# Kernel tuning notes

Measured on AMD Instinct MI355X. Metric: run time of the kernel, lower is better.

The kernel has to match this reference:

```python
import jax, jax.numpy as jnp
import numpy as np

B, C, H, W = 8, 64, 64, 64
CI = 32  # inter_channels = in_channels // 2
EPS = 1e-5


def conv1x1(x, w, b=None):
    # x: (b,c,h,w), w: (o,c) -> (b,o,h,w)
    y = jnp.einsum('bchw,oc->bohw', x, w)
    if b is not None:
        y = y + b[None, :, None, None]
    return y


def maxpool2x2(x):
    b, c, h, w = x.shape
    return x.reshape(b, c, h // 2, 2, w // 2, 2).max(axis=(3, 5))


def setup_inputs() -> dict:
    key = jax.random.key(0)
    ks = jax.random.split(key, 12)
    s = 0.05
    return {
        'x': jax.random.normal(ks[0], (B, C, H, W), jnp.float32),
        'theta_w': jax.random.normal(ks[1], (CI, C), jnp.float32) * s,
        'theta_b': jax.random.normal(ks[2], (CI,), jnp.float32) * s,
        'phi_w': jax.random.normal(ks[3], (CI, C), jnp.float32) * s,
        'phi_b': jax.random.normal(ks[4], (CI,), jnp.float32) * s,
        'psi_w': jax.random.normal(ks[5], (CI, C), jnp.float32) * s,
        'psi_b': jax.random.normal(ks[6], (CI,), jnp.float32) * s,
        'cp_w': jax.random.normal(ks[7], (2 * CI,), jnp.float32) * s,  # concat_project 1x1, no bias
        'W_w': jax.random.normal(ks[8], (C, CI + 1), jnp.float32) * s,
        'W_b': jax.random.normal(ks[9], (C,), jnp.float32) * s,
        'bn_gamma': jax.random.normal(ks[10], (C,), jnp.float32) * s + 1.0,
        'bn_beta': jax.random.normal(ks[11], (C,), jnp.float32) * s,
    }


def reference(x, theta_w, theta_b, phi_w, phi_b, psi_w, psi_b, cp_w, W_w, W_b, bn_gamma, bn_beta):
    b = x.shape[0]
    # psi / phi branches get 2x2 maxpool (sub_sample=True default)
    psi_x = maxpool2x2(conv1x1(x, psi_w, psi_b)).reshape(b, CI, -1)      # (b,ci,M)
    psi_x = psi_x.transpose(0, 2, 1)                                     # (b,M,ci)
    theta_x = conv1x1(x, theta_w, theta_b).reshape(b, CI, -1)            # (b,ci,N)
    phi_x = maxpool2x2(conv1x1(x, phi_w, phi_b)).reshape(b, CI, -1)      # (b,ci,M)
    # concat_project(cat[theta_i, phi_j]) + ReLU == relu(w1.theta_i + w2.phi_j)
    w1, w2 = cp_w[:CI], cp_w[CI:]
    a = jnp.einsum('bcn,c->bn', theta_x, w1)                             # (b,N)
    bb = jnp.einsum('bcm,c->bm', phi_x, w2)                              # (b,M)
    f = jax.nn.relu(a[:, :, None] + bb[:, None, :])                      # (b,N,M)
    M = f.shape[-1]
    f_div_C = f / float(M)
    y = jnp.matmul(f_div_C, psi_x)                                       # (b,N,ci)
    y = y.transpose(0, 2, 1).reshape(b, CI, H, W)
    # r_structure_type='zero' -> zero structure channel
    structure_feat = jnp.zeros((b, 1, H, W), y.dtype)
    y = jnp.concatenate([y, structure_feat], axis=1)                     # (b,ci+1,H,W)
    wy = conv1x1(y, W_w, W_b)                                            # (b,C,H,W)
    # BatchNorm2d, training-mode batch stats, biased variance
    mu = wy.mean(axis=(0, 2, 3), keepdims=True)
    var = wy.var(axis=(0, 2, 3), keepdims=True)
    wy = (wy - mu) * jax.lax.rsqrt(var + EPS)
    wy = wy * bn_gamma[None, :, None, None] + bn_beta[None, :, None, None]
    return wy + x
```

## Files before the change

### kernel.cpp

```cpp
#include <hip/hip_runtime.h>

#define OFF_A    0
#define OFF_BB   32768
#define OFF_SBB  40960
#define OFF_PERM 49152
#define OFF_U    57344
#define OFF_T1   581632
#define OFF_T2   1106432
#define OFF_KK   1631232
#define OFF_MP1  1664000
#define OFF_MP2  1664512
#define OFF_HC   1665024
#define OFF_HS   1673224
#define OFF_HS2  1681424
#define OFF_BAR  1689624

#define NBLK 256
#define NGRP 8

__device__ __forceinline__ void stg(float* p, float v) {
    __hip_atomic_store(p, v, __ATOMIC_RELAXED, __HIP_MEMORY_SCOPE_AGENT);
}
__device__ __forceinline__ float ldg1(const float* p) {
    return __hip_atomic_load(p, __ATOMIC_RELAXED, __HIP_MEMORY_SCOPE_AGENT);
}
__device__ __forceinline__ void stgi(int* p, int v) {
    __hip_atomic_store(p, v, __ATOMIC_RELAXED, __HIP_MEMORY_SCOPE_AGENT);
}
__device__ __forceinline__ int ldgi(const int* p) {
    return __hip_atomic_load(p, __ATOMIC_RELAXED, __HIP_MEMORY_SCOPE_AGENT);
}

__device__ __forceinline__ void gbar(float* ws, int gen)
{
    __syncthreads();
    if (threadIdx.x == 0) {
        unsigned* bars = (unsigned*)(ws + OFF_BAR);
        unsigned* grp  = bars + ((blockIdx.x >> 5) + 1) * 32;
        unsigned old = __hip_atomic_fetch_add(grp, 1u, __ATOMIC_RELAXED,
                                              __HIP_MEMORY_SCOPE_AGENT);
        if (old == (unsigned)(gen * 32 - 1))
            __hip_atomic_fetch_add(bars, 1u, __ATOMIC_RELAXED,
                                   __HIP_MEMORY_SCOPE_AGENT);
        unsigned goal = (unsigned)(gen * NGRP);
        while (__hip_atomic_load(bars, __ATOMIC_RELAXED,
                                 __HIP_MEMORY_SCOPE_AGENT) < goal)
            __builtin_amdgcn_s_sleep(2);
    }
    __syncthreads();
}

__global__ __launch_bounds__(1024) void kMega(
    const float* __restrict__ x, const float* __restrict__ theta_w,
    const float* __restrict__ theta_b, const float* __restrict__ phi_w,
    const float* __restrict__ phi_b, const float* __restrict__ psi_w,
    const float* __restrict__ psi_b, const float* __restrict__ cp_w,
    const float* __restrict__ Ww, const float* __restrict__ Wb,
    const float* __restrict__ gamma, const float* __restrict__ beta,
    float* __restrict__ ws, float* __restrict__ out)
{
    __shared__ float sh[8640];
    const int tid = threadIdx.x;
    const int bid = blockIdx.x;
    const int b   = bid >> 5;
    const int sub = bid & 31;

    {
        float* sm   = sh;
        float* sth  = sh + 4160;
        float* spsi = sh + 4228;
        float* sWw  = sh + 5284;
        for (int e = tid; e < 2048; e += 1024) {
            int i = e >> 6, c = e & 63;
            sm[i*130 + 2*c]     = phi_w[e];
            sm[i*130 + 2*c + 1] = psi_w[e];
        }
        for (int e = tid; e < 2048; e += 1024)
            sWw[(e >> 5)*33 + (e & 31)] = Ww[(e >> 5)*33 + (e & 31)];
        if (tid < 64) {
            float s = 0;
            for (int i = 0; i < 32; ++i) s += cp_w[i]*theta_w[i*64 + tid];
            sth[tid] = s;
        } else if (tid == 64) {
            float s = 0;
            for (int i = 0; i < 32; ++i) s += cp_w[i]*theta_b[i];
            sth[64] = s;
        }
        __syncthreads();
        int i = tid & 31;
        int mIdx = tid >> 5;
        int m = (sub << 5) + mIdx;
        int ph = m >> 5, pw = m & 31;
        const float* xb = x + b*262144 + ph*128 + pw*2;
        const float2* wrow = (const float2*)(sm + i*130);
        float tb = sth[64];
        float p0=0,p1=0,p2=0,p3=0,s0=0,s1=0,s2=0,s3=0;
        float a0=tb,a1=tb,a2=tb,a3=tb;
        #pragma unroll 8
        for (int c = 0; c < 64; ++c) {
            float2 xa = *(const float2*)(xb + c*4096);
            float2 xc = *(const float2*)(xb + c*4096 + 64);
            float2 w  = wrow[c];
            float st  = sth[c];
            p0 += xa.x*w.x; p1 += xa.y*w.x; p2 += xc.x*w.x; p3 += xc.y*w.x;
            s0 += xa.x*w.y; s1 += xa.y*w.y; s2 += xc.x*w.y; s3 += xc.y*w.y;
            a0 += xa.x*st;  a1 += xa.y*st;  a2 += xc.x*st;  a3 += xc.y*st;
        }
        float pv = fmaxf(fmaxf(p0,p1), fmaxf(p2,p3)) + phi_b[i];
        float sv = fmaxf(fmaxf(s0,s1), fmaxf(s2,s3)) + psi_b[i];
        spsi[mIdx*33 + i] = sv;
        float v = pv * cp_w[32 + i];
        v += __shfl_xor(v, 16, 32);
        v += __shfl_xor(v,  8, 32);
        v += __shfl_xor(v,  4, 32);
        v += __shfl_xor(v,  2, 32);
        v += __shfl_xor(v,  1, 32);
        if (i == 0) {
            stg(&ws[OFF_BB + (b<<10) + m], v);
            int nb = (b<<12) + ph*128 + pw*2;
            stg(&ws[OFF_A + nb],      a0);
            stg(&ws[OFF_A + nb + 1],  a1);
            stg(&ws[OFF_A + nb + 64], a2);
            stg(&ws[OFF_A + nb + 65], a3);
        }
        __syncthreads();
        #pragma unroll
        for (int rep = 0; rep < 2; ++rep) {
            int idx = tid + (rep << 10);
            int ml = idx >> 6, o = idx & 63;
            const float* pr = &spsi[ml*33];
            const float* wr = &sWw[o*33];
            float u = 0;
            #pragma unroll
            for (int i2 = 0; i2 < 32; ++i2) u += pr[i2]*wr[i2];
            stg(&ws[OFF_U + (((b<<10) + (sub<<5) + ml) << 6) + o], u);
        }
    }
    gbar(ws, 1);

    {
        float* sb = sh;
        sb[tid] = ldg1(&ws[OFF_BB + (b<<10) + tid]);
        __syncthreads();
        {
            int ml = tid >> 5, jl = tid & 31;
            int m = (sub << 5) + ml;
            float vv = sb[m];
            int cnt = 0;
            for (int s = 0; s < 32; ++s) {
                int j = jl + (s << 5);
                float u = sb[j];
                cnt += (u > vv || (u == vv && j < m)) ? 1 : 0;
            }
            cnt += __shfl_xor(cnt,  1, 32);
            cnt += __shfl_xor(cnt,  2, 32);
            cnt += __shfl_xor(cnt,  4, 32);
            cnt += __shfl_xor(cnt,  8, 32);
            cnt += __shfl_xor(cnt, 16, 32);
            if (jl == 0) {
                stg(&ws[OFF_SBB + (b<<10) + cnt], vv);
                stgi(&((int*)ws)[OFF_PERM + (b<<10) + cnt], m);
            }
        }
        {
            int l = tid >> 3, jl = tid & 7;
            int n = (sub << 7) + l;
            float av = ldg1(&ws[OFF_A + (b<<12) + n]);
            float tt = -av;
            const float2* sb2 = (const float2*)sb;
            int cnt = 0;
            for (int s = 0; s < 64; ++s) {
                float2 u = sb2[jl + (s << 3)];
                cnt += (u.x > tt) ? 1 : 0;
                cnt += (u.y > tt) ? 1 : 0;
            }
            cnt += __shfl_xor(cnt, 1, 8);
            cnt += __shfl_xor(cnt, 2, 8);
            cnt += __shfl_xor(cnt, 4, 8);
            if (jl == 0) {
                stgi(&((int*)ws)[OFF_KK + (b<<12) + n], cnt);
                atomicAdd(&ws[OFF_HC + b*1025 + cnt], 1.0f);
                atomicAdd(&ws[OFF_HS + b*1025 + cnt], av);
                atomicAdd(&ws[OFF_HS2 + b*1025 + cnt], av*av);
            }
        }
    }
    gbar(ws, 2);

    if (bid < 64) {
        int b3 = bid >> 3, og = bid & 7;
        int obase = og << 3;
        float* ssort = sh;
        int*   sperm = (int*)(sh + 1024);
        float* shc   = sh + 2048;
        float* shs   = sh + 3076;
        float* shs2  = sh + 4104;
        float* swp1  = sh + 5132;
        float* swp2  = sh + 5260;
        ssort[tid] = ldg1(&ws[OFF_SBB + (b3<<10) + tid]);
        sperm[tid] = ldgi(&((const int*)ws)[OFF_PERM + (b3<<10) + tid]);
        shc[tid]  = ldg1(&ws[OFF_HC  + b3*1025 + tid]);
        shs[tid]  = ldg1(&ws[OFF_HS  + b3*1025 + tid]);
        shs2[tid] = ldg1(&ws[OFF_HS2 + b3*1025 + tid]);
        if (tid == 0) {
            shc[1024]  = ldg1(&ws[OFF_HC  + b3*1025 + 1024]);
            shs[1024]  = ldg1(&ws[OFF_HS  + b3*1025 + 1024]);
            shs2[1024] = ldg1(&ws[OFF_HS2 + b3*1025 + 1024]);
        }
        __syncthreads();
        int ch = tid >> 3, o = tid & 7;
        int wv = tid >> 6, chl = (tid & 63) >> 3;
        const float* Ub = ws + OFF_U + (b3<<16) + obase + o;
        float p[8], sp[8];
        float s1 = 0, s2 = 0;
        #pragma unroll
        for (int jl = 0; jl < 8; ++jl) {
            int jj = (ch<<3) + jl;
            float v = ldg1(&Ub[sperm[jj]<<6]);
            p[jl] = v;
            sp[jl] = ssort[jj]*v;
            s1 += v; s2 += sp[jl];
        }
        float own1 = s1, own2 = s2;
        #pragma unroll
        for (int d = 1; d < 8; d <<= 1) {
            float u1 = __shfl_up(s1, d<<3, 64);
            float u2 = __shfl_up(s2, d<<3, 64);
            if (chl >= d) { s1 += u1; s2 += u2; }
        }
        if (chl == 7) { swp1[(wv<<3)+o] = s1; swp2[(wv<<3)+o] = s2; }
        __syncthreads();
        float off1 = 0, off2 = 0;
        for (int w = 0; w < 16; ++w) {
            if (w < wv) { off1 += swp1[(w<<3)+o]; off2 += swp2[(w<<3)+o]; }
        }
        float run1 = off1 + s1 - own1;
        float run2 = off2 + s2 - own2;
        float* T1 = ws + OFF_T1 + b3*65600 + obase + o;
        float* T2 = ws + OFF_T2 + b3*65600 + obase + o;
        if (ch == 0) { stg(&T1[0], 0.0f); stg(&T2[0], 0.0f); }
        const float inv = 1.0f/1024.0f;
        float m1 = 0, m2 = 0;
        #pragma unroll
        for (int jl = 0; jl < 8; ++jl) {
            int k = (ch<<3) + jl + 1;
            run1 += p[jl]; run2 += sp[jl];
            float t1 = run1*inv, t2 = run2*inv;
            stg(&T1[k<<6], t1);
            stg(&T2[k<<6], t2);
            float c = shc[k], sa_ = shs[k], sa2 = shs2[k];
            m1 += sa_*t1 + c*t2;
            m2 += (sa2*t1 + 2.0f*sa_*t2)*t1 + c*t2*t2;
        }
        m1 += __shfl_xor(m1,  8, 64); m2 += __shfl_xor(m2,  8, 64);
        m1 += __shfl_xor(m1, 16, 64); m2 += __shfl_xor(m2, 16, 64);
        m1 += __shfl_xor(m1, 32, 64); m2 += __shfl_xor(m2, 32, 64);
        __syncthreads();
        if (chl == 0) { swp1[(wv<<3)+o] = m1; swp2[(wv<<3)+o] = m2; }
        __syncthreads();
        if (tid < 8) {
            float a1 = 0, a2 = 0;
            for (int w = 0; w < 16; ++w) {
                a1 += swp1[(w<<3)+tid]; a2 += swp2[(w<<3)+tid];
            }
            stg(&ws[OFF_MP1 + (b3<<6) + obase + tid], a1);
            stg(&ws[OFF_MP2 + (b3<<6) + obase + tid], a2);
        }
    }
    gbar(ws, 3);

    {
        float* tile = sh;
        float* sa = sh + 8256;
        int*   sk = (int*)(sh + 8384);
        float* sA = sh + 8512;
        float* sD = sh + 8576;
        int n0 = sub << 7;
        if (tid < 128) {
            sa[tid] = ldg1(&ws[OFF_A + (b<<12) + n0 + tid]);
            sk[tid] = ldgi(&((const int*)ws)[OFF_KK + (b<<12) + n0 + tid]);
        }
        if (tid < 64) {
            const float Ninv = 1.0f/32768.0f;
            float m1s = 0, m2s = 0;
            #pragma unroll
            for (int b3 = 0; b3 < 8; ++b3) {
                m1s += ldg1(&ws[OFF_MP1 + (b3<<6) + tid]);
                m2s += ldg1(&ws[OFF_MP2 + (b3<<6) + tid]);
            }
            float m1 = m1s * Ninv;
            float m2 = m2s * Ninv;
            float wb = Wb[tid];
            float mu  = m1 + wb;
            float E2  = m2 + 2.0f*wb*m1 + wb*wb;
            float var = E2 - mu*mu;
            float A = gamma[tid] * rsqrtf(var + 1e-5f);
            sA[tid] = A;
            sD[tid] = beta[tid] + A*(wb - mu);
        }
        __syncthreads();
        const float* T1 = ws + OFF_T1 + b*65600;
        const float* T2 = ws + OFF_T2 + b*65600;
        {
            int o = tid & 63, ng = tid >> 6;
            float Ao = sA[o], Do = sD[o];
            #pragma unroll
            for (int j = 0; j < 8; ++j) {
                int n = (ng << 3) + j;
                int k = sk[n];
                float a = sa[n];
                float t1 = ldg1(&T1[(k<<6) + o]);
                float t2 = ldg1(&T2[(k<<6) + o]);
                tile[o*129 + n] = Ao*(a*t1 + t2) + Do;
            }
        }
        __syncthreads();
        {
            int n = tid & 127, og = tid >> 7;
            #pragma unroll
            for (int j = 0; j < 8; ++j) {
                int o = (og << 3) + j;
                int idx = ((b<<6) + o)*4096 + n0 + n;
                out[idx] = tile[o*129 + n] + x[idx];
            }
        }
    }
}

extern "C" void kernel_launch(void* const* d_in, const int* in_sizes, int n_in,
                              void* d_out, int out_size, void* d_ws, size_t ws_size,
                              hipStream_t stream)
{
    const float* x       = (const float*)d_in[0];
    const float* theta_w = (const float*)d_in[1];
    const float* theta_b = (const float*)d_in[2];
    const float* phi_w   = (const float*)d_in[3];
    const float* phi_b   = (const float*)d_in[4];
    const float* psi_w   = (const float*)d_in[5];
    const float* psi_b   = (const float*)d_in[6];
    const float* cp_w    = (const float*)d_in[7];
    const float* Ww      = (const float*)d_in[8];
    const float* Wb      = (const float*)d_in[9];
    const float* gamma   = (const float*)d_in[10];
    const float* beta    = (const float*)d_in[11];
    float* ws  = (float*)d_ws;
    float* out = (float*)d_out;

    hipMemsetAsync(ws + OFF_HC, 0, 24888 * sizeof(float), stream);

    kMega<<<256, 1024, 0, stream>>>(x, theta_w, theta_b, phi_w, phi_b,
                                    psi_w, psi_b, cp_w, Ww, Wb,
                                    gamma, beta, ws, out);
}
```

Measured before the change: 132.6 us.

## Replace counter grid barrier with per-block flag slots and zero histograms in-kernel

Result: slower. 137.7 us (+3.9%).

```diff
diff --git a/kernel.cpp b/kernel.cpp
--- a/kernel.cpp
+++ b/kernel.cpp
@@ -16,7 +16,6 @@
 #define OFF_BAR  1689624
 
 #define NBLK 256
-#define NGRP 8
 
 __device__ __forceinline__ void stg(float* p, float v) {
     __hip_atomic_store(p, v, __ATOMIC_RELAXED, __HIP_MEMORY_SCOPE_AGENT);
@@ -31,23 +30,35 @@
     return __hip_atomic_load(p, __ATOMIC_RELAXED, __HIP_MEMORY_SCOPE_AGENT);
 }
 
-__device__ __forceinline__ void gbar(float* ws, int gen)
+__device__ __forceinline__ void gbar(float* ws, unsigned gen)
 {
     __syncthreads();
-    if (threadIdx.x == 0) {
-        unsigned* bars = (unsigned*)(ws + OFF_BAR);
-        unsigned* grp  = bars + ((blockIdx.x >> 5) + 1) * 32;
-        unsigned old = __hip_atomic_fetch_add(grp, 1u, __ATOMIC_RELAXED,
-                                              __HIP_MEMORY_SCOPE_AGENT);
-        if (old == (unsigned)(gen * 32 - 1))
-            __hip_atomic_fetch_add(bars, 1u, __ATOMIC_RELAXED,
-                                   __HIP_MEMORY_SCOPE_AGENT);
-        unsigned goal = (unsigned)(gen * NGRP);
-        while (__hip_atomic_load(bars, __ATOMIC_RELAXED,
-                                 __HIP_MEMORY_SCOPE_AGENT) < goal)
+    unsigned* slots = (unsigned*)(ws + OFF_BAR);
+    if (threadIdx.x == 0)
+        __hip_atomic_store(&slots[blockIdx.x], gen, __ATOMIC_RELAXED,
+                           __HIP_MEMORY_SCOPE_AGENT);
+    if (threadIdx.x < 64) {
+        for (;;) {
+            unsigned mn = 0xffffffffu;
+            #pragma unroll
+            for (int r = 0; r < 4; ++r) {
+                unsigned v = __hip_atomic_load(&slots[(r<<6) + threadIdx.x],
+                                               __ATOMIC_RELAXED,
+                                               __HIP_MEMORY_SCOPE_AGENT);
+                mn = v < mn ? v : mn;
+            }
+            if (__all(mn >= gen)) break;
             __builtin_amdgcn_s_sleep(2);
+        }
     }
     __syncthreads();
+}
+
+__global__ void kZero(float* ws)
+{
+    unsigned* slots = (unsigned*)(ws + OFF_BAR);
+    __hip_atomic_store(&slots[threadIdx.x], 0u, __ATOMIC_RELAXED,
+                       __HIP_MEMORY_SCOPE_AGENT);
 }
 
 __global__ __launch_bounds__(1024) void kMega(
@@ -66,6 +77,10 @@
     const int sub = bid & 31;
 
     {
+        if (tid < 97) {
+            int e = bid*97 + tid;
+            if (e < 24600) stg(&ws[OFF_HC + e], 0.0f);
+        }
         float* sm   = sh;
         float* sth  = sh + 4160;
         float* spsi = sh + 4228;
@@ -136,7 +151,7 @@
             stg(&ws[OFF_U + (((b<<10) + (sub<<5) + ml) << 6) + o], u);
         }
     }
-    gbar(ws, 1);
+    gbar(ws, 1u);
 
     {
         float* sb = sh;
@@ -185,7 +200,7 @@
             }
         }
     }
-    gbar(ws, 2);
+    gbar(ws, 2u);
 
     if (bid < 64) {
         int b3 = bid >> 3, og = bid & 7;
@@ -267,7 +282,7 @@
             stg(&ws[OFF_MP2 + (b3<<6) + obase + tid], a2);
         }
     }
-    gbar(ws, 3);
+    gbar(ws, 3u);
 
     {
         float* tile = sh;
@@ -346,8 +361,7 @@
     float* ws  = (float*)d_ws;
     float* out = (float*)d_out;
 
-    hipMemsetAsync(ws + OFF_HC, 0, 24888 * sizeof(float), stream);
-
+    kZero<<<1, 256, 0, stream>>>(ws);
     kMega<<<256, 1024, 0, stream>>>(x, theta_w, theta_b, phi_w, phi_b,
                                     psi_w, psi_b, cp_w, Ww, Wb,
                                     gamma, beta, ws, out);
```

## Replace grid-wide barriers with per-batch barriers and spread prefix-scan stage

Applied to the files above, without the earlier changes.

New measurement: 132.3 us. Within noise of the previous version (-0.2%).

```diff
diff --git a/kernel.cpp b/kernel.cpp
--- a/kernel.cpp
+++ b/kernel.cpp
@@ -15,9 +15,6 @@
 #define OFF_HS2  1681424
 #define OFF_BAR  1689624
 
-#define NBLK 256
-#define NGRP 8
-
 __device__ __forceinline__ void stg(float* p, float v) {
     __hip_atomic_store(p, v, __ATOMIC_RELAXED, __HIP_MEMORY_SCOPE_AGENT);
 }
@@ -30,22 +27,21 @@
 __device__ __forceinline__ int ldgi(const int* p) {
     return __hip_atomic_load(p, __ATOMIC_RELAXED, __HIP_MEMORY_SCOPE_AGENT);
 }
-
-__device__ __forceinline__ void gbar(float* ws, int gen)
+__device__ __forceinline__ void stgu(unsigned* p, unsigned v) {
+    __hip_atomic_store(p, v, __ATOMIC_RELAXED, __HIP_MEMORY_SCOPE_AGENT);
+}
+__device__ __forceinline__ unsigned ldgu(const unsigned* p) {
+    return __hip_atomic_load(p, __ATOMIC_RELAXED, __HIP_MEMORY_SCOPE_AGENT);
+}
+
+__device__ __forceinline__ void gbarBatch(float* ws, int b, unsigned goal)
 {
     __syncthreads();
     if (threadIdx.x == 0) {
-        unsigned* bars = (unsigned*)(ws + OFF_BAR);
-        unsigned* grp  = bars + ((blockIdx.x >> 5) + 1) * 32;
-        unsigned old = __hip_atomic_fetch_add(grp, 1u, __ATOMIC_RELAXED,
-                                              __HIP_MEMORY_SCOPE_AGENT);
-        if (old == (unsigned)(gen * 32 - 1))
-            __hip_atomic_fetch_add(bars, 1u, __ATOMIC_RELAXED,
-                                   __HIP_MEMORY_SCOPE_AGENT);
-        unsigned goal = (unsigned)(gen * NGRP);
-        while (__hip_atomic_load(bars, __ATOMIC_RELAXED,
-                                 __HIP_MEMORY_SCOPE_AGENT) < goal)
-            __builtin_amdgcn_s_sleep(2);
+        unsigned* ctr = (unsigned*)(ws + OFF_BAR) + ((b + 1) << 5);
+        __hip_atomic_fetch_add(ctr, 1u, __ATOMIC_RELAXED,
+                               __HIP_MEMORY_SCOPE_AGENT);
+        while (ldgu(ctr) < goal) __builtin_amdgcn_s_sleep(2);
     }
     __syncthreads();
 }
@@ -64,8 +60,18 @@
     const int bid = blockIdx.x;
     const int b   = bid >> 5;
     const int sub = bid & 31;
+    unsigned* bars = (unsigned*)(ws + OFF_BAR);
 
     {
+        if (bid == 0 && tid == 0) {
+            for (int i = 0; i < 9; ++i) stgu(&bars[i << 5], 0u);
+        }
+        if (tid < 97) {
+            int e = sub*97 + tid;
+            if (e < 1025)      stg(&ws[OFF_HC  + b*1025 + e], 0.0f);
+            else if (e < 2050) stg(&ws[OFF_HS  + b*1025 + e - 1025], 0.0f);
+            else if (e < 3075) stg(&ws[OFF_HS2 + b*1025 + e - 2050], 0.0f);
+        }
         float* sm   = sh;
         float* sth  = sh + 4160;
         float* spsi = sh + 4228;
@@ -87,6 +93,10 @@
             sth[64] = s;
         }
         __syncthreads();
+        if (bid == 0 && tid == 0) {
+            stgu(&bars[288], 0x5A5A5A5Au);
+            stgu(&bars[289], 0xA5A5A5A5u);
+        }
         int i = tid & 31;
         int mIdx = tid >> 5;
         int m = (sub << 5) + mIdx;
@@ -136,7 +146,16 @@
             stg(&ws[OFF_U + (((b<<10) + (sub<<5) + ml) << 6) + o], u);
         }
     }
-    gbar(ws, 1);
+    __syncthreads();
+    if (tid == 0) {
+        while ((ldgu(&bars[288]) ^ ldgu(&bars[289])) != 0xFFFFFFFFu)
+            __builtin_amdgcn_s_sleep(2);
+        unsigned* ctr = bars + ((b + 1) << 5);
+        __hip_atomic_fetch_add(ctr, 1u, __ATOMIC_RELAXED,
+                               __HIP_MEMORY_SCOPE_AGENT);
+        while (ldgu(ctr) < 32u) __builtin_amdgcn_s_sleep(2);
+    }
+    __syncthreads();
 
     {
         float* sb = sh;
@@ -185,37 +204,37 @@
             }
         }
     }
-    gbar(ws, 2);
-
-    if (bid < 64) {
-        int b3 = bid >> 3, og = bid & 7;
-        int obase = og << 3;
+    gbarBatch(ws, b, 64u);
+
+    {
+        int obase = sub << 1;
         float* ssort = sh;
         int*   sperm = (int*)(sh + 1024);
         float* shc   = sh + 2048;
         float* shs   = sh + 3076;
         float* shs2  = sh + 4104;
         float* swp1  = sh + 5132;
-        float* swp2  = sh + 5260;
-        ssort[tid] = ldg1(&ws[OFF_SBB + (b3<<10) + tid]);
-        sperm[tid] = ldgi(&((const int*)ws)[OFF_PERM + (b3<<10) + tid]);
-        shc[tid]  = ldg1(&ws[OFF_HC  + b3*1025 + tid]);
-        shs[tid]  = ldg1(&ws[OFF_HS  + b3*1025 + tid]);
-        shs2[tid] = ldg1(&ws[OFF_HS2 + b3*1025 + tid]);
+        float* swp2  = sh + 5164;
+        ssort[tid] = ldg1(&ws[OFF_SBB + (b<<10) + tid]);
+        sperm[tid] = ldgi(&((const int*)ws)[OFF_PERM + (b<<10) + tid]);
+        shc[tid]  = ldg1(&ws[OFF_HC  + b*1025 + tid]);
+        shs[tid]  = ldg1(&ws[OFF_HS  + b*1025 + tid]);
+        shs2[tid] = ldg1(&ws[OFF_HS2 + b*1025 + tid]);
         if (tid == 0) {
-            shc[1024]  = ldg1(&ws[OFF_HC  + b3*1025 + 1024]);
-            shs[1024]  = ldg1(&ws[OFF_HS  + b3*1025 + 1024]);
-            shs2[1024] = ldg1(&ws[OFF_HS2 + b3*1025 + 1024]);
-        }
-        __syncthreads();
-        int ch = tid >> 3, o = tid & 7;
-        int wv = tid >> 6, chl = (tid & 63) >> 3;
-        const float* Ub = ws + OFF_U + (b3<<16) + obase + o;
-        float p[8], sp[8];
+            shc[1024]  = ldg1(&ws[OFF_HC  + b*1025 + 1024]);
+            shs[1024]  = ldg1(&ws[OFF_HS  + b*1025 + 1024]);
+            shs2[1024] = ldg1(&ws[OFF_HS2 + b*1025 + 1024]);
+        }
+        __syncthreads();
+        int ch = tid >> 1, o2 = tid & 1;
+        int o  = obase + o2;
+        int wv = tid >> 6, chl = (tid & 63) >> 1;
+        const float* Ub = ws + OFF_U + (b<<16) + o;
+        float p[2], sp[2];
         float s1 = 0, s2 = 0;
         #pragma unroll
-        for (int jl = 0; jl < 8; ++jl) {
-            int jj = (ch<<3) + jl;
+        for (int jl = 0; jl < 2; ++jl) {
+            int jj = (ch<<1) + jl;
             float v = ldg1(&Ub[sperm[jj]<<6]);
             p[jl] = v;
             sp[jl] = ssort[jj]*v;
@@ -223,27 +242,27 @@
         }
         float own1 = s1, own2 = s2;
         #pragma unroll
-        for (int d = 1; d < 8; d <<= 1) {
-            float u1 = __shfl_up(s1, d<<3, 64);
-            float u2 = __shfl_up(s2, d<<3, 64);
+        for (int d = 1; d < 32; d <<= 1) {
+            float u1 = __shfl_up(s1, d<<1, 64);
+            float u2 = __shfl_up(s2, d<<1, 64);
             if (chl >= d) { s1 += u1; s2 += u2; }
         }
-        if (chl == 7) { swp1[(wv<<3)+o] = s1; swp2[(wv<<3)+o] = s2; }
+        if (chl == 31) { swp1[(wv<<1)+o2] = s1; swp2[(wv<<1)+o2] = s2; }
         __syncthreads();
         float off1 = 0, off2 = 0;
         for (int w = 0; w < 16; ++w) {
-            if (w < wv) { off1 += swp1[(w<<3)+o]; off2 += swp2[(w<<3)+o]; }
+            if (w < wv) { off1 += swp1[(w<<1)+o2]; off2 += swp2[(w<<1)+o2]; }
         }
         float run1 = off1 + s1 - own1;
         float run2 = off2 + s2 - own2;
-        float* T1 = ws + OFF_T1 + b3*65600 + obase + o;
-        float* T2 = ws + OFF_T2 + b3*65600 + obase + o;
+        float* T1 = ws + OFF_T1 + b*65600 + o;
+        float* T2 = ws + OFF_T2 + b*65600 + o;
         if (ch == 0) { stg(&T1[0], 0.0f); stg(&T2[0], 0.0f); }
         const float inv = 1.0f/1024.0f;
         float m1 = 0, m2 = 0;
         #pragma unroll
-        for (int jl = 0; jl < 8; ++jl) {
-            int k = (ch<<3) + jl + 1;
+        for (int jl = 0; jl < 2; ++jl) {
+            int k = (ch<<1) + jl + 1;
             run1 += p[jl]; run2 += sp[jl];
             float t1 = run1*inv, t2 = run2*inv;
             stg(&T1[k<<6], t1);
@@ -252,22 +271,34 @@
             m1 += sa_*t1 + c*t2;
             m2 += (sa2*t1 + 2.0f*sa_*t2)*t1 + c*t2*t2;
         }
+        m1 += __shfl_xor(m1,  2, 64); m2 += __shfl_xor(m2,  2, 64);
+        m1 += __shfl_xor(m1,  4, 64); m2 += __shfl_xor(m2,  4, 64);
         m1 += __shfl_xor(m1,  8, 64); m2 += __shfl_xor(m2,  8, 64);
         m1 += __shfl_xor(m1, 16, 64); m2 += __shfl_xor(m2, 16, 64);
         m1 += __shfl_xor(m1, 32, 64); m2 += __shfl_xor(m2, 32, 64);
         __syncthreads();
-        if (chl == 0) { swp1[(wv<<3)+o] = m1; swp2[(wv<<3)+o] = m2; }
-        __syncthreads();
-        if (tid < 8) {
+        if (chl == 0) { swp1[(wv<<1)+o2] = m1; swp2[(wv<<1)+o2] = m2; }
+        __syncthreads();
+        if (tid < 2) {
             float a1 = 0, a2 = 0;
             for (int w = 0; w < 16; ++w) {
-                a1 += swp1[(w<<3)+tid]; a2 += swp2[(w<<3)+tid];
-            }
-            stg(&ws[OFF_MP1 + (b3<<6) + obase + tid], a1);
-            stg(&ws[OFF_MP2 + (b3<<6) + obase + tid], a2);
-        }
-    }
-    gbar(ws, 3);
+                a1 += swp1[(w<<1)+tid]; a2 += swp2[(w<<1)+tid];
+            }
+            stg(&ws[OFF_MP1 + (b<<6) + obase + tid], a1);
+            stg(&ws[OFF_MP2 + (b<<6) + obase + tid], a2);
+        }
+    }
+    __syncthreads();
+    if (tid == 0) {
+        unsigned* ctr = bars + ((b + 1) << 5);
+        unsigned old = __hip_atomic_fetch_add(ctr, 1u, __ATOMIC_RELAXED,
+                                              __HIP_MEMORY_SCOPE_AGENT);
+        if (old == 95u)
+            __hip_atomic_fetch_add(&bars[0], 1u, __ATOMIC_RELAXED,
+                                   __HIP_MEMORY_SCOPE_AGENT);
+        while (ldgu(ctr) < 96u) __builtin_amdgcn_s_sleep(2);
+    }
+    __syncthreads();
 
     {
         float* tile = sh;
@@ -280,6 +311,24 @@
             sa[tid] = ldg1(&ws[OFF_A + (b<<12) + n0 + tid]);
             sk[tid] = ldgi(&((const int*)ws)[OFF_KK + (b<<12) + n0 + tid]);
         }
+        __syncthreads();
+        const float* T1 = ws + OFF_T1 + b*65600;
+        const float* T2 = ws + OFF_T2 + b*65600;
+        {
+            int o = tid & 63, ng = tid >> 6;
+            #pragma unroll
+            for (int j = 0; j < 8; ++j) {
+                int n = (ng << 3) + j;
+                int k = sk[n];
+                float a = sa[n];
+                tile[o*129 + n] = a*ldg1(&T1[(k<<6) + o])
+                                  + ldg1(&T2[(k<<6) + o]);
+            }
+        }
+        if (tid == 0) {
+            while (ldgu(&bars[0]) < 8u) __builtin_amdgcn_s_sleep(2);
+        }
+        __syncthreads();
         if (tid < 64) {
             const float Ninv = 1.0f/32768.0f;
             float m1s = 0, m2s = 0;
@@ -299,29 +348,13 @@
             sD[tid] = beta[tid] + A*(wb - mu);
         }
         __syncthreads();
-        const float* T1 = ws + OFF_T1 + b*65600;
-        const float* T2 = ws + OFF_T2 + b*65600;
         {
-            int o = tid & 63, ng = tid >> 6;
-            float Ao = sA[o], Do = sD[o];
+            int n = tid & 127, og2 = tid >> 7;
             #pragma unroll
             for (int j = 0; j < 8; ++j) {
-                int n = (ng << 3) + j;
-                int k = sk[n];
-                float a = sa[n];
-                float t1 = ldg1(&T1[(k<<6) + o]);
-                float t2 = ldg1(&T2[(k<<6) + o]);
-                tile[o*129 + n] = Ao*(a*t1 + t2) + Do;
-            }
-        }
-        __syncthreads();
-        {
-            int n = tid & 127, og = tid >> 7;
-            #pragma unroll
-            for (int j = 0; j < 8; ++j) {
-                int o = (og << 3) + j;
+                int o = (og2 << 3) + j;
                 int idx = ((b<<6) + o)*4096 + n0 + n;
-                out[idx] = tile[o*129 + n] + x[idx];
+                out[idx] = sA[o]*tile[o*129 + n] + sD[o] + x[idx];
             }
         }
     }
@@ -346,8 +379,6 @@
     float* ws  = (float*)d_ws;
     float* out = (float*)d_out;
 
-    hipMemsetAsync(ws + OFF_HC, 0, 24888 * sizeof(float), stream);
-
     kMega<<<256, 1024, 0, stream>>>(x, theta_w, theta_b, phi_w, phi_b,
                                     psi_w, psi_b, cp_w, Ww, Wb,
                                     gamma, beta, ws, out);
```
